# Kernel optimization log

Measured on AMD Instinct MI355X. Metric: run time of the kernel, lower is better.

## Reference

```python
import jax, jax.numpy as jnp
import numpy as np

HEADS = 8

def conv1x1(x, w, b=None):
    # x: [b,c,h,w], w: [o,c]
    y = jnp.einsum('bchw,oc->bohw', x, w)
    if b is not None:
        y = y + b[None, :, None, None]
    return y

def dwconv3(x, w):
    # depthwise 3x3, SAME padding; w: [C,1,3,3]
    return jax.lax.conv_general_dilated(
        x, w, window_strides=(1, 1), padding='SAME',
        feature_group_count=x.shape[1],
        dimension_numbers=('NCHW', 'OIHW', 'NCHW'))

def layernorm_c(x, w, b):
    # WithBias LayerNorm over channel dim (torch normalizes last dim of b,(hw),c)
    mu = x.mean(axis=1, keepdims=True)
    var = ((x - mu) ** 2).mean(axis=1, keepdims=True)
    return (x - mu) / jnp.sqrt(var + 1e-5) * w[None, :, None, None] + b[None, :, None, None]

def l2norm_lastdim(x):
    n = jnp.sqrt(jnp.sum(x * x, axis=-1, keepdims=True))
    return x / jnp.maximum(n, 1e-12)

def channel_attention(xq, xkv, q_w, q_dw_w, kv_w, kv_dw_w, temperature, attn4, proj_w):
    b, c, h, w = xq.shape
    q = dwconv3(conv1x1(xq, q_w), q_dw_w)
    kv = dwconv3(conv1x1(xkv, kv_w), kv_dw_w)
    k, v = jnp.split(kv, 2, axis=1)
    ch = c // HEADS  # channels per head
    def heads(t):
        return t.reshape(b, HEADS, ch, h * w)
    q, k, v = heads(q), heads(k), heads(v)
    q = l2norm_lastdim(q)
    k = l2norm_lastdim(k)
    attn = jnp.einsum('bhcn,bhdn->bhcd', q, k) * temperature[None]  # [b,H,ch,ch]
    kk = int(ch * 0.9)
    thr = jax.lax.top_k(attn, kk)[0][..., -1:]
    masked = jnp.where(attn >= thr, attn, -jnp.inf)
    score = jax.nn.softmax(masked, axis=-1)
    out = jnp.einsum('bhcd,bhdn->bhcn', score, v) * attn4
    out = out.reshape(b, c, h, w)
    return conv1x1(out, proj_w)

def geglu_ffn(x, ffn_in_w, ffn_dw_w, ffn_out_w):
    y = conv1x1(x, ffn_in_w)
    y = dwconv3(y, ffn_dw_w)
    y1, y2 = jnp.split(y, 2, axis=1)
    return conv1x1(jax.nn.gelu(y1, approximate=False) * y2, ffn_out_w)


def reference(vi_featur, ir_featur, text_code,
              se_w1, se_w2, conv1x1_w, conv1x1_b, conv_out_w, conv_out_b,
              text_w1, text_b1, text_w2, text_b2,
              norm1_w, norm1_b, norm2_w, norm2_b, norm3_w, norm3_b,
              q_w, q_dw_w, kv_w, kv_dw_w, temperature, attn4, proj_w,
              ffn_in_w, ffn_dw_w, ffn_out_w):
    b, c, h, w = vi_featur.shape
    concat = jnp.concatenate([vi_featur, ir_featur], axis=1)  # [b,2c,h,w]
    squeeze = concat.mean(axis=(2, 3))                         # [b,2c]
    cw = jax.nn.sigmoid(jax.nn.relu(squeeze @ se_w1.T) @ se_w2.T)
    topk = c  # int(2*ch_dim*0.5)
    idx = jax.lax.top_k(cw, topk)[1]                           # [b,topk]
    selected = jnp.take_along_axis(concat, idx[:, :, None, None], axis=1)
    img = conv1x1(selected, conv1x1_w, conv1x1_b)              # [b,2c,h,w]
    tf = jax.nn.relu(text_code @ text_w1.T + text_b1) @ text_w2.T + text_b2  # [b,2c]
    soft_idx = jax.lax.top_k(tf, 2 * c)[1]                     # full descending perm
    shuffled = jnp.take_along_axis(img, soft_idx[:, :, None, None], axis=1)
    q_in = conv1x1(shuffled, conv_out_w, conv_out_b)           # [b,c,h,w]
    img_feature2 = conv1x1(concat, conv_out_w, conv_out_b)
    att = channel_attention(layernorm_c(q_in, norm1_w, norm1_b),
                            layernorm_c(img_feature2, norm2_w, norm2_b),
                            q_w, q_dw_w, kv_w, kv_dw_w, temperature, attn4, proj_w)
    output = att + geglu_ffn(layernorm_c(att, norm3_w, norm3_b), ffn_in_w, ffn_dw_w, ffn_out_w)
    return (output, img_feature2)


def setup_inputs() -> dict:
    key = jax.random.key(0)
    ks = jax.random.split(key, 20)
    B, C, H, W = 4, 128, 128, 128
    s = 0.05
    d = {
        'vi_featur': jax.random.normal(ks[0], (B, C, H, W), jnp.float32),
        'ir_featur': jax.random.normal(ks[1], (B, C, H, W), jnp.float32),
        'text_code': jax.random.normal(ks[2], (B, 512), jnp.float32),
        'se_w1': jax.random.normal(ks[3], (32, 256), jnp.float32) * s,
        'se_w2': jax.random.normal(ks[4], (256, 32), jnp.float32) * s,
        'conv1x1_w': jax.random.normal(ks[5], (256, 128), jnp.float32) * s,
        'conv1x1_b': jnp.zeros((256,), jnp.float32),
        'conv_out_w': jax.random.normal(ks[6], (128, 256), jnp.float32) * s,
        'conv_out_b': jnp.zeros((128,), jnp.float32),
        'text_w1': jax.random.normal(ks[7], (512, 512), jnp.float32) * s,
        'text_b1': jnp.zeros((512,), jnp.float32),
        'text_w2': jax.random.normal(ks[8], (256, 512), jnp.float32) * s,
        'text_b2': jnp.zeros((256,), jnp.float32),
        'norm1_w': jnp.ones((128,), jnp.float32), 'norm1_b': jnp.zeros((128,), jnp.float32),
        'norm2_w': jnp.ones((128,), jnp.float32), 'norm2_b': jnp.zeros((128,), jnp.float32),
        'norm3_w': jnp.ones((128,), jnp.float32), 'norm3_b': jnp.zeros((128,), jnp.float32),
        'q_w': jax.random.normal(ks[9], (128, 128), jnp.float32) * s,
        'q_dw_w': jax.random.normal(ks[10], (128, 1, 3, 3), jnp.float32) * s,
        'kv_w': jax.random.normal(ks[11], (256, 128), jnp.float32) * s,
        'kv_dw_w': jax.random.normal(ks[12], (256, 1, 3, 3), jnp.float32) * s,
        'temperature': jnp.ones((8, 1, 1), jnp.float32),
        'attn4': jnp.ones((1,), jnp.float32) * 0.2,
        'proj_w': jax.random.normal(ks[13], (128, 128), jnp.float32) * s,
        'ffn_in_w': jax.random.normal(ks[14], (680, 128), jnp.float32) * s,
        'ffn_dw_w': jax.random.normal(ks[15], (680, 1, 3, 3), jnp.float32) * s,
        'ffn_out_w': jax.random.normal(ks[16], (128, 340), jnp.float32) * s,
    }
    return d
```

## Files before the change

kernel.cpp:

```cpp
#include <hip/hip_runtime.h>

typedef unsigned short u16;
typedef __attribute__((ext_vector_type(8))) short bf16x8;
typedef __attribute__((ext_vector_type(4))) float f32x4;

#define N_PIX 16384
static constexpr long NP = 4L * 128 * N_PIX;

__device__ __forceinline__ float bf2f(u16 h) {
  unsigned u = ((unsigned)h) << 16; float f; __builtin_memcpy(&f, &u, 4); return f;
}
__device__ __forceinline__ u16 f2bf(float f) {
  unsigned u; __builtin_memcpy(&u, &f, 4);
  u = (u + 0x7fffu + ((u >> 16) & 1u)) >> 16; return (u16)u;
}

__device__ __forceinline__ float blockReduceSum256(float v) {
  #pragma unroll
  for (int o = 32; o > 0; o >>= 1) v += __shfl_down(v, o, 64);
  __shared__ float sw[4];
  int lane = threadIdx.x & 63, w = threadIdx.x >> 6;
  if (lane == 0) sw[w] = v;
  __syncthreads();
  return (threadIdx.x == 0) ? (sw[0] + sw[1] + sw[2] + sw[3]) : 0.f;
}

__global__ __launch_bounds__(256) void wconv5_k(const float* __restrict__ a0, u16* __restrict__ o0, long n0,
                                                const float* __restrict__ a1, u16* __restrict__ o1, long n1,
                                                const float* __restrict__ a2, u16* __restrict__ o2, long n2,
                                                const float* __restrict__ a3, u16* __restrict__ o3, long n3,
                                                const float* __restrict__ a4, u16* __restrict__ o4, long n4) {
  long i = (long)blockIdx.x * 256 + threadIdx.x;
  if (i < n0) o0[i] = f2bf(a0[i]);
  if (i < n1) o1[i] = f2bf(a1[i]);
  if (i < n2) o2[i] = f2bf(a2[i]);
  if (i < n3) o3[i] = f2bf(a3[i]);
  if (i < n4) o4[i] = f2bf(a4[i]);
}

__global__ __launch_bounds__(256) void squeeze_k(const float* __restrict__ vi,
                                                 const float* __restrict__ ir,
                                                 float* __restrict__ sq,
                                                 u16* __restrict__ cbf) {
  int c = blockIdx.x, b = blockIdx.y, tid = threadIdx.x;
  const float* src = (c < 128) ? (vi + ((long)b * 128 + c) * N_PIX)
                               : (ir + ((long)b * 128 + (c - 128)) * N_PIX);
  const f32x4* src4 = (const f32x4*)src;
  u16* dst = cbf + ((long)b * 256 + c) * N_PIX;
  float s = 0.f;
  #pragma unroll
  for (int j = 0; j < 8; ++j) {
    f32x4 v0 = src4[j * 512 + tid * 2];
    f32x4 v1 = src4[j * 512 + tid * 2 + 1];
    s += v0.x + v0.y + v0.z + v0.w + v1.x + v1.y + v1.z + v1.w;
    bf16x8 r;
    r[0] = (short)f2bf(v0.x); r[1] = (short)f2bf(v0.y);
    r[2] = (short)f2bf(v0.z); r[3] = (short)f2bf(v0.w);
    r[4] = (short)f2bf(v1.x); r[5] = (short)f2bf(v1.y);
    r[6] = (short)f2bf(v1.z); r[7] = (short)f2bf(v1.w);
    *(bf16x8*)(dst + j * 2048 + tid * 8) = r;
  }
  float t = blockReduceSum256(s);
  if (tid == 0) sq[b * 256 + c] = t * (1.f / 16384.f);
}

__global__ __launch_bounds__(256) void se_text1_k(const float* __restrict__ sq,
                                                  const float* __restrict__ sew1,
                                                  const float* __restrict__ sew2,
                                                  int* __restrict__ idx,
                                                  const float* __restrict__ tc,
                                                  const float* __restrict__ tw1,
                                                  const float* __restrict__ tb1,
                                                  float* __restrict__ t1f) {
  int b = blockIdx.y, tid = threadIdx.x;
  __shared__ float sm[544];
  if (blockIdx.x == 64) {
    float* s_sq = sm; float* s_h1 = sm + 256; float* s_cw = sm + 288;
    s_sq[tid] = sq[b * 256 + tid];
    __syncthreads();
    if (tid < 32) {
      float s = 0.f;
      for (int c = 0; c < 256; ++c) s += s_sq[c] * sew1[tid * 256 + c];
      s_h1[tid] = fmaxf(s, 0.f);
    }
    __syncthreads();
    {
      float s = 0.f;
      #pragma unroll
      for (int j = 0; j < 32; ++j) s += s_h1[j] * sew2[tid * 32 + j];
      s_cw[tid] = 1.f / (1.f + expf(-s));
    }
    __syncthreads();
    float my = s_cw[tid];
    int rk = 0;
    for (int c = 0; c < 256; ++c) {
      float o = s_cw[c];
      rk += (o > my) || (o == my && c < tid);
    }
    if (rk < 128) idx[b * 128 + rk] = tid;
  } else {
    float* s_tc = sm;
    int j0 = blockIdx.x * 8;
    s_tc[tid] = tc[b * 512 + tid];
    s_tc[tid + 256] = tc[b * 512 + 256 + tid];
    __syncthreads();
    int w = tid >> 6, lane = tid & 63;
    #pragma unroll
    for (int r = 0; r < 2; ++r) {
      int j = j0 + w * 2 + r;
      const float* wr = tw1 + (long)j * 512;
      float s = 0.f;
      #pragma unroll
      for (int k = 0; k < 8; ++k) s += s_tc[lane + k * 64] * wr[lane + k * 64];
      #pragma unroll
      for (int o = 32; o > 0; o >>= 1) s += __shfl_down(s, o, 64);
      if (lane == 0) t1f[b * 512 + j] = fmaxf(s + tb1[j], 0.f);
    }
  }
}

__global__ __launch_bounds__(256) void text2_k(const float* __restrict__ t1f,
                                               const float* __restrict__ tw2,
                                               const float* __restrict__ tb2,
                                               float* __restrict__ tf) {
  int b = blockIdx.y, j0 = blockIdx.x * 8, tid = threadIdx.x;
  __shared__ float s_t1[512];
  s_t1[tid] = t1f[b * 512 + tid];
  s_t1[tid + 256] = t1f[b * 512 + 256 + tid];
  __syncthreads();
  int w = tid >> 6, lane = tid & 63;
  #pragma unroll
  for (int r = 0; r < 2; ++r) {
    int j = j0 + w * 2 + r;
    const float* wr = tw2 + (long)j * 512;
    float s = 0.f;
    #pragma unroll
    for (int k = 0; k < 8; ++k) s += s_t1[lane + k * 64] * wr[lane + k * 64];
    #pragma unroll
    for (int o = 32; o > 0; o >>= 1) s += __shfl_down(s, o, 64);
    if (lane == 0) tf[b * 256 + j] = s + tb2[j];
  }
}

__global__ __launch_bounds__(256) void rank2_k(const float* __restrict__ tf,
                                               int* __restrict__ sidx) {
  int b = blockIdx.x, tid = threadIdx.x;
  __shared__ float s_tf[256];
  s_tf[tid] = tf[b * 256 + tid];
  __syncthreads();
  float my = s_tf[tid];
  int rk = 0;
  for (int c = 0; c < 256; ++c) {
    float o = s_tf[c];
    rk += (o > my) || (o == my && c < tid);
  }
  sidx[b * 256 + rk] = tid;
}

__global__ __launch_bounds__(128) void mcomb_k(const float* __restrict__ w2,
                                               const float* __restrict__ w2b,
                                               const float* __restrict__ w1,
                                               const float* __restrict__ w1b,
                                               const int* __restrict__ idx,
                                               const int* __restrict__ sidx,
                                               u16* __restrict__ mch,
                                               u16* __restrict__ mcl,
                                               float* __restrict__ bcomb) {
  int o = blockIdx.x, b = blockIdx.y, tid = threadIdx.x;
  __shared__ float s_w2[256];
  __shared__ int s_sx[256];
  s_w2[tid] = w2[o * 256 + tid];
  s_w2[tid + 128] = w2[o * 256 + tid + 128];
  s_sx[tid] = sidx[b * 256 + tid] & 255;
  s_sx[tid + 128] = sidx[b * 256 + tid + 128] & 255;
  u16* hrow = mch + ((long)b * 128 + o) * 256;
  u16* lrow = mcl + ((long)b * 128 + o) * 256;
  hrow[tid] = 0; hrow[tid + 128] = 0;
  lrow[tid] = 0; lrow[tid + 128] = 0;
  __syncthreads();
  float s = 0.f;
  for (int j = 0; j < 256; ++j) s += s_w2[j] * w1[s_sx[j] * 128 + tid];
  int cc = idx[b * 128 + tid] & 255;
  u16 hi = f2bf(s);
  hrow[cc] = hi;
  lrow[cc] = f2bf(s - bf2f(hi));
  if (tid == 0) {
    float bb = w2b[o];
    for (int j = 0; j < 256; ++j) bb += s_w2[j] * w1b[s_sx[j]];
    bcomb[b * 128 + o] = bb;
  }
}

__global__ __launch_bounds__(256) void gemm_dual_k(
    const u16* __restrict__ W2b, const float* __restrict__ b2,
    const u16* __restrict__ Mch, const u16* __restrict__ Mcl,
    const float* __restrict__ bc, const u16* __restrict__ Xb,
    float* __restrict__ out1, u16* __restrict__ xqT, u16* __restrict__ xkvT,
    const float* __restrict__ g1, const float* __restrict__ b1,
    const float* __restrict__ g2, const float* __restrict__ b2n) {
  const int N = N_PIX;
  int n0 = blockIdx.x * 64, bz = blockIdx.z, tid = threadIdx.x;
  __shared__ __align__(16) char smem[36864];
  u16* A1  = (u16*)smem;
  u16* A2h = (u16*)(smem + 9216);
  u16* A2l = (u16*)(smem + 18432);
  u16* Xs  = (u16*)(smem + 27648);
  __shared__ float gs1[128], bs1[128], gs2[128], bs2[128];
  if (tid < 128) { gs1[tid] = g1[tid]; bs1[tid] = b1[tid]; gs2[tid] = g2[tid]; bs2[tid] = b2n[tid]; }
  f32x4 acc1[2][4], acc2[2][4];
  #pragma unroll
  for (int ot = 0; ot < 2; ++ot)
    #pragma unroll
    for (int i = 0; i < 4; ++i) { acc1[ot][i] = (f32x4){0,0,0,0}; acc2[ot][i] = (f32x4){0,0,0,0}; }
  int wv = tid >> 6, lane = tid & 63;
  int lr = lane & 15, lkq = (lane >> 4) * 8;
  for (int kt = 0; kt < 4; ++kt) {
    int k0 = kt << 6;
    {
      int n = tid & 63;
      const u16* src = Xb + (long)bz * 256 * N + n0 + n;
      #pragma unroll
      for (int cc = 0; cc < 2; ++cc) {
        int kb = ((tid >> 6) << 3) + cc * 32;
        int k = k0 + kb;
        bf16x8 t;
        #pragma unroll
        for (int i = 0; i < 8; ++i) t[i] = (short)src[(long)(k + i) * N];
        *(bf16x8*)&Xs[n * 72 + kb] = t;
      }
    }
    #pragma unroll
    for (int ot = 0; ot < 2; ++ot) {
      {
        int r = tid >> 2, o = ot * 64 + r;
        #pragma unroll
        for (int cc = 0; cc < 2; ++cc) {
          int col = ((tid & 3) << 3) + cc * 32;
          int k = k0 + col;
          *(bf16x8*)&A1[r * 72 + col] = *(const bf16x8*)(W2b + (long)o * 256 + k);
          *(bf16x8*)&A2h[r * 72 + col] = *(const bf16x8*)(Mch + ((long)bz * 128 + o) * 256 + k);
          *(bf16x8*)&A2l[r * 72 + col] = *(const bf16x8*)(Mcl + ((long)bz * 128 + o) * 256 + k);
        }
      }
      __syncthreads();
      #pragma unroll
      for (int kk = 0; kk < 2; ++kk) {
        int lk = kk * 32 + lkq;
        bf16x8 a1 = *(const bf16x8*)&A1[(wv * 16 + lr) * 72 + lk];
        bf16x8 a2h = *(const bf16x8*)&A2h[(wv * 16 + lr) * 72 + lk];
        bf16x8 a2l = *(const bf16x8*)&A2l[(wv * 16 + lr) * 72 + lk];
        #pragma unroll
        for (int nt = 0; nt < 4; ++nt) {
          bf16x8 bfr = *(const bf16x8*)&Xs[(nt * 16 + lr) * 72 + lk];
          acc1[ot][nt] = __builtin_amdgcn_mfma_f32_16x16x32_bf16(a1, bfr, acc1[ot][nt], 0, 0, 0);
          acc2[ot][nt] = __builtin_amdgcn_mfma_f32_16x16x32_bf16(a2h, bfr, acc2[ot][nt], 0, 0, 0);
          acc2[ot][nt] = __builtin_amdgcn_mfma_f32_16x16x32_bf16(a2l, bfr, acc2[ot][nt], 0, 0, 0);
        }
      }
      __syncthreads();
    }
  }
  float* st1 = (float*)smem;
  #pragma unroll
  for (int ot = 0; ot < 2; ++ot) {
    #pragma unroll
    for (int nt = 0; nt < 4; ++nt)
      #pragma unroll
      for (int r4 = 0; r4 < 4; ++r4) {
        int o_l = wv * 16 + (lane >> 4) * 4 + r4;
        int n_l = nt * 16 + (lane & 15);
        st1[o_l * 68 + n_l] = acc1[ot][nt][r4] + b2[ot * 64 + o_l];
      }
    __syncthreads();
    {
      int row = tid >> 2, colb = (tid & 3) * 16;
      float* dst = out1 + ((long)bz * 128 + ot * 64 + row) * N + n0 + colb;
      #pragma unroll
      for (int j = 0; j < 4; ++j)
        *(f32x4*)(dst + j * 4) = *(f32x4*)&st1[row * 68 + colb + j * 4];
    }
    __syncthreads();
  }
  u16* stq = (u16*)smem;
  #pragma unroll
  for (int ot = 0; ot < 2; ++ot)
    #pragma unroll
    for (int nt = 0; nt < 4; ++nt)
      #pragma unroll
      for (int r4 = 0; r4 < 4; ++r4) {
        int o_a = ot * 64 + wv * 16 + (lane >> 4) * 4 + r4;
        int n_l = nt * 16 + (lane & 15);
        stq[n_l * 136 + o_a] = f2bf(acc2[ot][nt][r4] + bc[bz * 128 + o_a]);
      }
  __syncthreads();
  {
    int n = tid >> 2, c0 = (tid & 3) * 32;
    bf16x8 v[4];
    float sum = 0.f, sq = 0.f;
    #pragma unroll
    for (int j = 0; j < 4; ++j) {
      v[j] = *(const bf16x8*)&stq[n * 136 + c0 + j * 8];
      #pragma unroll
      for (int i = 0; i < 8; ++i) { float f = bf2f((u16)v[j][i]); sum += f; sq += f * f; }
    }
    sum += __shfl_xor(sum, 1, 64); sum += __shfl_xor(sum, 2, 64);
    sq  += __shfl_xor(sq, 1, 64);  sq  += __shfl_xor(sq, 2, 64);
    float mu = sum * (1.f / 128.f);
    float var = sq * (1.f / 128.f) - mu * mu;
    float rs = rsqrtf(fmaxf(var, 0.f) + 1e-5f);
    u16* dst = xqT + ((long)bz * N_PIX + n0 + n) * 128 + c0;
    #pragma unroll
    for (int j = 0; j < 4; ++j) {
      bf16x8 r;
      #pragma unroll
      for (int i = 0; i < 8; ++i) {
        float f = bf2f((u16)v[j][i]);
        r[i] = (short)f2bf((f - mu) * rs * gs1[c0 + j * 8 + i] + bs1[c0 + j * 8 + i]);
      }
      *(bf16x8*)(dst + j * 8) = r;
    }
  }
  __syncthreads();
  #pragma unroll
  for (int ot = 0; ot < 2; ++ot)
    #pragma unroll
    for (int nt = 0; nt < 4; ++nt)
      #pragma unroll
      for (int r4 = 0; r4 < 4; ++r4) {
        int o_a = ot * 64 + wv * 16 + (lane >> 4) * 4 + r4;
        int n_l = nt * 16 + (lane & 15);
        stq[n_l * 136 + o_a] = f2bf(acc1[ot][nt][r4] + b2[o_a]);
      }
  __syncthreads();
  {
    int n = tid >> 2, c0 = (tid & 3) * 32;
    bf16x8 v[4];
    float sum = 0.f, sq = 0.f;
    #pragma unroll
    for (int j = 0; j < 4; ++j) {
      v[j] = *(const bf16x8*)&stq[n * 136 + c0 + j * 8];
      #pragma unroll
      for (int i = 0; i < 8; ++i) { float f = bf2f((u16)v[j][i]); sum += f; sq += f * f; }
    }
    sum += __shfl_xor(sum, 1, 64); sum += __shfl_xor(sum, 2, 64);
    sq  += __shfl_xor(sq, 1, 64);  sq  += __shfl_xor(sq, 2, 64);
    float mu = sum * (1.f / 128.f);
    float var = sq * (1.f / 128.f) - mu * mu;
    float rs = rsqrtf(fmaxf(var, 0.f) + 1e-5f);
    u16* dst = xkvT + ((long)bz * N_PIX + n0 + n) * 128 + c0;
    #pragma unroll
    for (int j = 0; j < 4; ++j) {
      bf16x8 r;
      #pragma unroll
      for (int i = 0; i < 8; ++i) {
        float f = bf2f((u16)v[j][i]);
        r[i] = (short)f2bf((f - mu) * rs * gs2[c0 + j * 8 + i] + bs2[c0 + j * 8 + i]);
      }
      *(bf16x8*)(dst + j * 8) = r;
    }
  }
}

__global__ __launch_bounds__(256) void att_ln_k(
    const u16* __restrict__ Ah, const u16* __restrict__ Alo,
    const u16* __restrict__ V, long v_bstride,
    u16* __restrict__ att, u16* __restrict__ x3T,
    const float* __restrict__ g3, const float* __restrict__ b3) {
  const int N = N_PIX;
  int n0 = blockIdx.x * 64, bz = blockIdx.z, tid = threadIdx.x;
  int wv = tid >> 6, lane = tid & 63;
  int lr = lane & 15, lkq = (lane >> 4) * 8;
  __shared__ __align__(16) u16 Xs[64][136];
  __shared__ __align__(16) u16 As[64][136];
  __shared__ __align__(16) u16 Al[64][136];
  __shared__ float gs[128], bs[128];
  if (tid < 128) { gs[tid] = g3[tid]; bs[tid] = b3[tid]; }
  f32x4 acc[2][4];
  #pragma unroll
  for (int ot = 0; ot < 2; ++ot)
    #pragma unroll
    for (int i = 0; i < 4; ++i) acc[ot][i] = (f32x4){0.f, 0.f, 0.f, 0.f};
  {
    int n = tid & 63;
    const u16* src = V + (long)bz * v_bstride + n0 + n;
    #pragma unroll
    for (int cc = 0; cc < 4; ++cc) {
      int kb = ((tid >> 6) << 3) + cc * 32;
      bf16x8 t;
      #pragma unroll
      for (int i = 0; i < 8; ++i) t[i] = (short)src[(long)(kb + i) * N];
      *(bf16x8*)&Xs[n][kb] = t;
    }
  }
  #pragma unroll
  for (int ot = 0; ot < 2; ++ot) {
    {
      int r = tid >> 2, o = ot * 64 + r;
      #pragma unroll
      for (int cc = 0; cc < 4; ++cc) {
        int col = ((tid & 3) << 3) + cc * 32;
        long base = (long)bz * (128L * 128) + (long)o * 128 + col;
        *(bf16x8*)&As[r][col] = *(const bf16x8*)(Ah + base);
        *(bf16x8*)&Al[r][col] = *(const bf16x8*)(Alo + base);
      }
    }
    __syncthreads();
    #pragma unroll
    for (int kk = 0; kk < 4; ++kk) {
      int lk = kk * 32 + lkq;
      bf16x8 afr = *(const bf16x8*)&As[wv * 16 + lr][lk];
      bf16x8 alr = *(const bf16x8*)&Al[wv * 16 + lr][lk];
      #pragma unroll
      for (int nt = 0; nt < 4; ++nt) {
        bf16x8 bfr = *(const bf16x8*)&Xs[nt * 16 + lr][lk];
        acc[ot][nt] = __builtin_amdgcn_mfma_f32_16x16x32_bf16(afr, bfr, acc[ot][nt], 0, 0, 0);
        acc[ot][nt] = __builtin_amdgcn_mfma_f32_16x16x32_bf16(alr, bfr, acc[ot][nt], 0, 0, 0);
      }
    }
    __syncthreads();
  }
  u16* st = &Xs[0][0];
  #pragma unroll
  for (int ot = 0; ot < 2; ++ot) {
    #pragma unroll
    for (int nt = 0; nt < 4; ++nt)
      #pragma unroll
      for (int r4 = 0; r4 < 4; ++r4) {
        int row = wv * 16 + (lane >> 4) * 4 + r4;
        int col = nt * 16 + (lane & 15);
        st[row * 72 + col] = f2bf(acc[ot][nt][r4]);
      }
    __syncthreads();
    #pragma unroll
    for (int it = 0; it < 2; ++it) {
      int row = (tid >> 3) + it * 32;
      int col = (tid & 7) * 8;
      bf16x8 v = *(bf16x8*)&st[row * 72 + col];
      *(bf16x8*)(att + ((long)bz * 128 + ot * 64 + row) * N + n0 + col) = v;
    }
    __syncthreads();
  }
  u16* stq = &Xs[0][0];
  #pragma unroll
  for (int ot = 0; ot < 2; ++ot)
    #pragma unroll
    for (int nt = 0; nt < 4; ++nt)
      #pragma unroll
      for (int r4 = 0; r4 < 4; ++r4) {
        int o_a = ot * 64 + wv * 16 + (lane >> 4) * 4 + r4;
        int n_l = nt * 16 + (lane & 15);
        stq[n_l * 136 + o_a] = f2bf(acc[ot][nt][r4]);
      }
  __syncthreads();
  {
    int n = tid >> 2, c0 = (tid & 3) * 32;
    bf16x8 v[4];
    float sum = 0.f, sq = 0.f;
    #pragma unroll
    for (int j = 0; j < 4; ++j) {
      v[j] = *(const bf16x8*)&stq[n * 136 + c0 + j * 8];
      #pragma unroll
      for (int i = 0; i < 8; ++i) { float f = bf2f((u16)v[j][i]); sum += f; sq += f * f; }
    }
    sum += __shfl_xor(sum, 1, 64); sum += __shfl_xor(sum, 2, 64);
    sq  += __shfl_xor(sq, 1, 64);  sq  += __shfl_xor(sq, 2, 64);
    float mu = sum * (1.f / 128.f);
    float var = sq * (1.f / 128.f) - mu * mu;
    float rs = rsqrtf(fmaxf(var, 0.f) + 1e-5f);
    u16* dst = x3T + ((long)bz * N_PIX + n0 + n) * 128 + c0;
    #pragma unroll
    for (int j = 0; j < 4; ++j) {
      bf16x8 r;
      #pragma unroll
      for (int i = 0; i < 8; ++i) {
        float f = bf2f((u16)v[j][i]);
        r[i] = (short)f2bf((f - mu) * rs * gs[c0 + j * 8 + i] + bs[c0 + j * 8 + i]);
      }
      *(bf16x8*)(dst + j * 8) = r;
    }
  }
}

template<int AMODE, int RESADD, int OUTF, int XT, int OT>
__global__ __launch_bounds__(256) void gemm_k(
    const u16* __restrict__ Ah, const u16* __restrict__ Alo, long a_bstride,
    const u16* __restrict__ X, long x_bstride,
    const u16* __restrict__ res, long res_bstride,
    void* __restrict__ outv, long out_bstride,
    int O, int K) {
  const int N = N_PIX;
  int n0 = blockIdx.x * 64;
  int o0 = blockIdx.y * 64 * OT;
  int bz = blockIdx.z;
  int tid = threadIdx.x;
  int wv = tid >> 6, lane = tid & 63;
  int lr = lane & 15, lkq = (lane >> 4) * 8;
  __shared__ __align__(16) u16 Xs[64][136];
  __shared__ __align__(16) u16 As[(XT == 3) ? 1 : 64][136];
  f32x4 acc[OT][4];
  #pragma unroll
  for (int ot = 0; ot < OT; ++ot)
    #pragma unroll
    for (int i = 0; i < 4; ++i) acc[ot][i] = (f32x4){0.f, 0.f, 0.f, 0.f};

  if (XT == 3) {
    {
      int n = tid >> 2, koff = (tid & 3) << 5;
      const u16* src = X + (long)bz * x_bstride + (long)(n0 + n) * 128 + koff;
      #pragma unroll
      for (int j = 0; j < 4; ++j)
        *(bf16x8*)&Xs[n][koff + j * 8] = *(const bf16x8*)(src + j * 8);
    }
    __syncthreads();
    #pragma unroll
    for (int ot = 0; ot < OT; ++ot) {
      int oc = o0 + ot * 64 + wv * 16 + lr;
      if (oc > O - 1) oc = O - 1;
      const u16* Arow = Ah + (long)oc * 128;
      bf16x8 afr[4];
      #pragma unroll
      for (int kk = 0; kk < 4; ++kk) afr[kk] = *(const bf16x8*)(Arow + kk * 32 + lkq);
      #pragma unroll
      for (int kk = 0; kk < 4; ++kk) {
        int lk = kk * 32 + lkq;
        #pragma unroll
        for (int nt = 0; nt < 4; ++nt) {
          bf16x8 bfr = *(const bf16x8*)&Xs[nt * 16 + lr][lk];
          acc[ot][nt] = __builtin_amdgcn_mfma_f32_16x16x32_bf16(afr[kk], bfr, acc[ot][nt], 0, 0, 0);
        }
      }
    }
    __syncthreads();
  } else {
    int nk = (K + 127) >> 7;
    for (int kt = 0; kt < nk; ++kt) {
      int k0 = kt << 7;
      {
        int n = tid & 63;
        const u16* src = X + (long)bz * x_bstride + n0 + n;
        #pragma unroll
        for (int cc = 0; cc < 4; ++cc) {
          int kb = ((tid >> 6) << 3) + cc * 32;
          int k = k0 + kb;
          bf16x8 t;
          #pragma unroll
          for (int i = 0; i < 8; ++i)
            t[i] = (short)((k + i < K) ? src[(long)(k + i) * N] : (u16)0);
          *(bf16x8*)&Xs[n][kb] = t;
        }
      }
      #pragma unroll
      for (int ot = 0; ot < OT; ++ot) {
        {
          int r = tid >> 2, o = o0 + ot * 64 + r;
          #pragma unroll
          for (int cc = 0; cc < 4; ++cc) {
            int col = ((tid & 3) << 3) + cc * 32;
            int k = k0 + col;
            bf16x8 t;
            if (o < O && k + 8 <= K) {
              t = *(const bf16x8*)(Ah + (long)o * K + k);
            } else {
              #pragma unroll
              for (int i = 0; i < 8; ++i)
                t[i] = (short)((o < O && k + i < K) ? Ah[(long)o * K + k + i] : (u16)0);
            }
            *(bf16x8*)&As[r][col] = t;
          }
        }
        __syncthreads();
        #pragma unroll
        for (int kk = 0; kk < 4; ++kk) {
          int lk = kk * 32 + lkq;
          bf16x8 afr = *(const bf16x8*)&As[wv * 16 + lr][lk];
          #pragma unroll
          for (int nt = 0; nt < 4; ++nt) {
            bf16x8 bfr = *(const bf16x8*)&Xs[nt * 16 + lr][lk];
            acc[ot][nt] = __builtin_amdgcn_mfma_f32_16x16x32_bf16(afr, bfr, acc[ot][nt], 0, 0, 0);
          }
        }
        __syncthreads();
      }
    }
  }

  #pragma unroll
  for (int ot = 0; ot < OT; ++ot) {
    if (ot > 0) __syncthreads();
    if (OUTF == 0) {
      u16* st = &Xs[0][0];
      #pragma unroll
      for (int nt = 0; nt < 4; ++nt)
        #pragma unroll
        for (int r4 = 0; r4 < 4; ++r4) {
          int row = wv * 16 + (lane >> 4) * 4 + r4;
          int col = nt * 16 + (lane & 15);
          st[row * 72 + col] = f2bf(acc[ot][nt][r4]);
        }
      __syncthreads();
      #pragma unroll
      for (int it = 0; it < 2; ++it) {
        int row = (tid >> 3) + it * 32;
        int col = (tid & 7) * 8;
        int o = o0 + ot * 64 + row;
        if (o < O) {
          bf16x8 v = *(bf16x8*)&st[row * 72 + col];
          *(bf16x8*)((u16*)outv + (long)bz * out_bstride + (long)o * N + n0 + col) = v;
        }
      }
    } else {
      float* st = (float*)&Xs[0][0];
      #pragma unroll
      for (int nt = 0; nt < 4; ++nt)
        #pragma unroll
        for (int r4 = 0; r4 < 4; ++r4) {
          int row = wv * 16 + (lane >> 4) * 4 + r4;
          int col = nt * 16 + (lane & 15);
          st[row * 68 + col] = acc[ot][nt][r4];
        }
      __syncthreads();
      {
        int row = tid >> 2, colb = (tid & 3) * 16;
        int o = o0 + ot * 64 + row;
        if (o < O) {
          float* dst = (float*)outv + (long)bz * out_bstride + (long)o * N + n0 + colb;
          bf16x8 rv0, rv1;
          if (RESADD) {
            const u16* rp = res + (long)bz * res_bstride + (long)o * N + n0 + colb;
            rv0 = *(const bf16x8*)rp;
            rv1 = *(const bf16x8*)(rp + 8);
          }
          #pragma unroll
          for (int j = 0; j < 4; ++j) {
            f32x4 v = *(f32x4*)&st[row * 68 + colb + j * 4];
            if (RESADD) {
              #pragma unroll
              for (int i = 0; i < 4; ++i) {
                int idx = j * 4 + i;
                u16 rr = (u16)((idx < 8) ? rv0[idx] : rv1[idx - 8]);
                v[i] += bf2f(rr);
              }
            }
            *(f32x4*)(dst + j * 4) = v;
          }
        }
      }
    }
  }
}

__global__ __launch_bounds__(256) void dw3t2_k(const u16* __restrict__ inQ,
                                               const float* __restrict__ wQ,
                                               u16* __restrict__ outQ,
                                               const u16* __restrict__ inKV,
                                               const float* __restrict__ wKV,
                                               u16* __restrict__ outKV) {
  int gp = blockIdx.x >> 3, stripe = blockIdx.x & 7, tid = threadIdx.x;
  const u16* in; const float* w; u16* out; int c; long pbase;
  if (gp < 512) { in = inQ;  w = wQ;  out = outQ;  c = gp & 127;  pbase = (long)gp * N_PIX; }
  else { int p2 = gp - 512; in = inKV; w = wKV; out = outKV; c = p2 & 255; pbase = (long)p2 * N_PIX; }
  int y0 = stripe * 16;
  __shared__ __align__(16) u16 tile[18][136];
  for (int v = tid; v < 288; v += 256) {
    int r = v >> 4, col = (v & 15) << 3;
    int y = y0 - 1 + r;
    bf16x8 t;
    #pragma unroll
    for (int i = 0; i < 8; ++i) t[i] = 0;
    if (y >= 0 && y < 128) t = *(const bf16x8*)(in + pbase + y * 128 + col);
    *(bf16x8*)&tile[r][col] = t;
  }
  float wv[9];
  #pragma unroll
  for (int j = 0; j < 9; ++j) wv[j] = w[c * 9 + j];
  __syncthreads();
  int row = tid >> 4, col0 = (tid & 15) << 3;
  float a[3][10];
  #pragma unroll
  for (int dr = 0; dr < 3; ++dr)
    #pragma unroll
    for (int i = 0; i < 10; ++i) {
      int x = col0 - 1 + i;
      a[dr][i] = (x >= 0 && x < 128) ? bf2f(tile[row + dr][x]) : 0.f;
    }
  bf16x8 res;
  #pragma unroll
  for (int j = 0; j < 8; ++j) {
    float s = 0.f;
    #pragma unroll
    for (int dr = 0; dr < 3; ++dr)
      #pragma unroll
      for (int dx = 0; dx < 3; ++dx) s += wv[dr * 3 + dx] * a[dr][j + dx];
    res[j] = (short)f2bf(s);
  }
  *(bf16x8*)(out + pbase + (y0 + row) * 128 + col0) = res;
}

__global__ __launch_bounds__(256) void dw3gelu4_k(const u16* __restrict__ ft,
                                                  const float* __restrict__ w,
                                                  u16* __restrict__ fg) {
  int plane = blockIdx.x >> 3, stripe = blockIdx.x & 7, tid = threadIdx.x;
  int b = plane / 340, c = plane % 340;
  const u16* t1 = ft + ((long)b * 680 + c) * N_PIX;
  const u16* t2 = ft + ((long)b * 680 + 340 + c) * N_PIX;
  u16* g = fg + ((long)b * 340 + c) * N_PIX;
  int y0 = stripe * 16;
  __shared__ __align__(16) u16 ta[18][136];
  __shared__ __align__(16) u16 tb[18][136];
  for (int v = tid; v < 288; v += 256) {
    int r = v >> 4, col = (v & 15) << 3;
    int y = y0 - 1 + r;
    bf16x8 u1, u2;
    #pragma unroll
    for (int i = 0; i < 8; ++i) { u1[i] = 0; u2[i] = 0; }
    if (y >= 0 && y < 128) {
      u1 = *(const bf16x8*)(t1 + y * 128 + col);
      u2 = *(const bf16x8*)(t2 + y * 128 + col);
    }
    *(bf16x8*)&ta[r][col] = u1;
    *(bf16x8*)&tb[r][col] = u2;
  }
  float w1[9], w2[9];
  #pragma unroll
  for (int j = 0; j < 9; ++j) { w1[j] = w[c * 9 + j]; w2[j] = w[(340 + c) * 9 + j]; }
  __syncthreads();
  int row = tid >> 4, col0 = (tid & 15) << 3;
  float a[3][10], bb[3][10];
  #pragma unroll
  for (int dr = 0; dr < 3; ++dr)
    #pragma unroll
    for (int i = 0; i < 10; ++i) {
      int x = col0 - 1 + i;
      bool ok = (x >= 0 && x < 128);
      a[dr][i] = ok ? bf2f(ta[row + dr][x]) : 0.f;
      bb[dr][i] = ok ? bf2f(tb[row + dr][x]) : 0.f;
    }
  bf16x8 res;
  #pragma unroll
  for (int j = 0; j < 8; ++j) {
    float s1 = 0.f, s2 = 0.f;
    #pragma unroll
    for (int dr = 0; dr < 3; ++dr)
      #pragma unroll
      for (int dx = 0; dx < 3; ++dx) {
        s1 += w1[dr * 3 + dx] * a[dr][j + dx];
        s2 += w2[dr * 3 + dx] * bb[dr][j + dx];
      }
    float gl = 0.5f * s1 * (1.f + erff(s1 * 0.70710678118f));
    res[j] = (short)f2bf(gl * s2);
  }
  *(bf16x8*)(g + (y0 + row) * 128 + col0) = res;
}

__global__ __launch_bounds__(256) void rownorm2_k(const u16* __restrict__ q,
                                                  const u16* __restrict__ kv,
                                                  float* __restrict__ qn,
                                                  float* __restrict__ kn) {
  int x = blockIdx.x, b = blockIdx.y, tid = threadIdx.x;
  const u16* src;
  float* dst;
  if (x < 128) { src = q + (long)b * 128 * N_PIX + (long)x * N_PIX; dst = qn + b * 128 + x; }
  else { int r = x - 128; src = kv + (long)b * 256 * N_PIX + (long)r * N_PIX; dst = kn + b * 128 + r; }
  float s = 0.f;
  #pragma unroll
  for (int j = 0; j < 8; ++j) {
    bf16x8 v = *(const bf16x8*)(src + j * 2048 + tid * 8);
    #pragma unroll
    for (int i = 0; i < 8; ++i) { float f = bf2f((u16)v[i]); s += f * f; }
  }
  float t = blockReduceSum256(s);
  if (tid == 0) *dst = sqrtf(t);
}

__global__ __launch_bounds__(256) void attn_part_k(const u16* __restrict__ q,
                                                   const u16* __restrict__ kbase,
                                                   long kbstride,
                                                   float* __restrict__ part) {
  int ch = blockIdx.x, h = blockIdx.y, b = blockIdx.z, tid = threadIdx.x;
  int n0 = ch * 256;
  __shared__ __align__(16) u16 qc[16][280];
  __shared__ __align__(16) u16 kc[16][280];
  #pragma unroll
  for (int j = 0; j < 2; ++j) {
    int v = tid + j * 256;
    int r = v >> 5, col = (v & 31) << 3;
    *(bf16x8*)&qc[r][col] = *(const bf16x8*)(q + ((long)b * 128 + h * 16 + r) * N_PIX + n0 + col);
    *(bf16x8*)&kc[r][col] = *(const bf16x8*)(kbase + (long)b * kbstride + (long)(h * 16 + r) * N_PIX + n0 + col);
  }
  __syncthreads();
  int c = tid >> 4, d = tid & 15;
  float acc = 0.f;
  #pragma unroll 4
  for (int nb = 0; nb < 32; ++nb) {
    bf16x8 qv = *(const bf16x8*)&qc[c][nb * 8];
    bf16x8 kv = *(const bf16x8*)&kc[d][nb * 8];
    #pragma unroll
    for (int i = 0; i < 8; ++i) acc += bf2f((u16)qv[i]) * bf2f((u16)kv[i]);
  }
  part[(long)((((b * 8 + h) * 16 + c) * 16 + d)) * 64 + ch] = acc;
}

__global__ __launch_bounds__(256) void attn_reduce_k(const float* __restrict__ part,
                                                     const float* __restrict__ qn,
                                                     const float* __restrict__ kn,
                                                     const float* __restrict__ temp,
                                                     float* __restrict__ attnm) {
  int idx = blockIdx.x * 256 + threadIdx.x;
  const float* p = part + (long)idx * 64;
  float s = 0.f;
  #pragma unroll
  for (int j = 0; j < 64; ++j) s += p[j];
  int d = idx & 15, c = (idx >> 4) & 15, h = (idx >> 8) & 7, b = idx >> 11;
  float nq = fmaxf(qn[b * 128 + h * 16 + c], 1e-12f);
  float nk = fmaxf(kn[b * 128 + h * 16 + d], 1e-12f);
  attnm[idx] = s / (nq * nk) * temp[h];
}

__global__ __launch_bounds__(128) void score_cmb_k(const float* __restrict__ attnm,
                                                   const float* __restrict__ projw,
                                                   const float* __restrict__ attn4p,
                                                   u16* __restrict__ cmbh,
                                                   u16* __restrict__ cmbl) {
  int b = blockIdx.x, tid = threadIdx.x;
  __shared__ float att_s[2048], score_s[2048];
  for (int i = tid; i < 2048; i += 128) att_s[i] = attnm[(long)b * 2048 + i];
  __syncthreads();
  {
    int h = tid >> 4, c = tid & 15;
    float v[16], t[16];
    #pragma unroll
    for (int d = 0; d < 16; ++d) { v[d] = att_s[(h * 16 + c) * 16 + d]; t[d] = v[d]; }
    float thr = 0.f, M = -1e30f;
    for (int it = 0; it < 14; ++it) {
      float m = -1e30f; int mi = 0;
      #pragma unroll
      for (int d = 0; d < 16; ++d) if (t[d] > m) { m = t[d]; mi = d; }
      if (it == 0) M = m;
      thr = m;
      t[mi] = -1e31f;
    }
    float s = 0.f, e[16];
    #pragma unroll
    for (int d = 0; d < 16; ++d) { e[d] = (v[d] >= thr) ? expf(v[d] - M) : 0.f; s += e[d]; }
    float inv = 1.f / s;
    #pragma unroll
    for (int d = 0; d < 16; ++d) score_s[(h * 16 + c) * 16 + d] = e[d] * inv;
  }
  __syncthreads();
  float a4 = attn4p[0];
  int o = tid;
  for (int hd = 0; hd < 128; ++hd) {
    int h = hd >> 4, d = hd & 15;
    float s = 0.f;
    #pragma unroll
    for (int c = 0; c < 16; ++c)
      s += projw[o * 128 + h * 16 + c] * score_s[(h * 16 + c) * 16 + d];
    float v = a4 * s;
    long oi = ((long)b * 128 + o) * 128 + hd;
    u16 hi = f2bf(v);
    cmbh[oi] = hi;
    cmbl[oi] = f2bf(v - bf2f(hi));
  }
}

extern "C" void kernel_launch(void* const* d_in, const int* in_sizes, int n_in,
                              void* d_out, int out_size, void* d_ws, size_t ws_size,
                              hipStream_t stream) {
  (void)in_sizes; (void)n_in; (void)out_size; (void)ws_size;
  const float* vi        = (const float*)d_in[0];
  const float* ir        = (const float*)d_in[1];
  const float* text_code = (const float*)d_in[2];
  const float* se_w1     = (const float*)d_in[3];
  const float* se_w2     = (const float*)d_in[4];
  const float* conv1x1_w = (const float*)d_in[5];
  const float* conv1x1_b = (const float*)d_in[6];
  const float* conv_out_w= (const float*)d_in[7];
  const float* conv_out_b= (const float*)d_in[8];
  const float* text_w1   = (const float*)d_in[9];
  const float* text_b1   = (const float*)d_in[10];
  const float* text_w2   = (const float*)d_in[11];
  const float* text_b2   = (const float*)d_in[12];
  const float* norm1_w   = (const float*)d_in[13];
  const float* norm1_b   = (const float*)d_in[14];
  const float* norm2_w   = (const float*)d_in[15];
  const float* norm2_b   = (const float*)d_in[16];
  const float* norm3_w   = (const float*)d_in[17];
  const float* norm3_b   = (const float*)d_in[18];
  const float* q_w       = (const float*)d_in[19];
  const float* q_dw_w    = (const float*)d_in[20];
  const float* kv_w      = (const float*)d_in[21];
  const float* kv_dw_w   = (const float*)d_in[22];
  const float* temperature = (const float*)d_in[23];
  const float* attn4     = (const float*)d_in[24];
  const float* proj_w    = (const float*)d_in[25];
  const float* ffn_in_w  = (const float*)d_in[26];
  const float* ffn_dw_w  = (const float*)d_in[27];
  const float* ffn_out_w = (const float*)d_in[28];
  float* out0 = (float*)d_out;
  float* out1 = out0 + NP;

  char* W = (char*)d_ws;
  float* sq_f  = (float*)(W + 0);
  int*   idx_i = (int*)(W + 4096);
  int*   sidx_i= (int*)(W + 6144);
  u16*   Mch   = (u16*)(W + 12288);
  u16*   Mcl   = (u16*)(W + 274432);
  float* bcomb = (float*)(W + 536576);
  float* qn_f  = (float*)(W + 538624);
  float* kn_f  = (float*)(W + 540672);
  float* attnm = (float*)(W + 542720);
  u16*   cmbh  = (u16*)(W + 575488);
  u16*   cmbl  = (u16*)(W + 706560);
  float* t1f   = (float*)(W + 834560);
  float* tf_f  = (float*)(W + 842752);
  u16*   W2b   = (u16*)(W + 846848);
  u16*   qwb   = (u16*)(W + 912384);
  u16*   kvwb  = (u16*)(W + 945152);
  u16*   ffnWb = (u16*)(W + (1 << 20));
  u16*   ffnOb = (u16*)(W + (1 << 20) + 174080);
  u16* S    = (u16*)(W + (2 << 20));
  u16* CC   = S;
  u16* KD   = S + 512L * N_PIX;
  u16* KVD  = S + 1024L * N_PIX;
  u16* CBF  = S + 1024L * N_PIX;
  u16* X3T  = S + 2048L * N_PIX;
  u16* XKVT = S + 2560L * N_PIX;
  u16* FT4  = S + 2560L * N_PIX;
  u16* FG4  = S + 5280L * N_PIX;
  u16* KVT  = (u16*)out0;
  u16* ATT  = KD;

  const long SN = 128L * N_PIX;
  const long SN2 = 256L * N_PIX;

  wconv5_k<<<340, 256, 0, stream>>>(conv_out_w, W2b, 32768, q_w, qwb, 16384,
                                    kv_w, kvwb, 32768, ffn_in_w, ffnWb, 87040,
                                    ffn_out_w, ffnOb, 43520);
  squeeze_k<<<dim3(256, 4), 256, 0, stream>>>(vi, ir, sq_f, CBF);
  se_text1_k<<<dim3(65, 4), 256, 0, stream>>>(sq_f, se_w1, se_w2, idx_i,
                                              text_code, text_w1, text_b1, t1f);
  text2_k<<<dim3(32, 4), 256, 0, stream>>>(t1f, text_w2, text_b2, tf_f);
  rank2_k<<<4, 256, 0, stream>>>(tf_f, sidx_i);
  mcomb_k<<<dim3(128, 4), 128, 0, stream>>>(conv_out_w, conv_out_b, conv1x1_w,
                                            conv1x1_b, idx_i, sidx_i, Mch, Mcl, bcomb);
  gemm_dual_k<<<dim3(256, 1, 4), 256, 0, stream>>>(
      W2b, conv_out_b, Mch, Mcl, bcomb, CBF, out1, CC, XKVT,
      norm1_w, norm1_b, norm2_w, norm2_b);
  gemm_k<2, 0, 0, 3, 2><<<dim3(256, 1, 4), 256, 0, stream>>>(
      qwb, nullptr, 0, CC, SN, nullptr, 0, KD, SN, 128, 128);
  gemm_k<2, 0, 0, 3, 2><<<dim3(256, 2, 4), 256, 0, stream>>>(
      kvwb, nullptr, 0, XKVT, SN, nullptr, 0, KVT, SN2, 256, 128);
  dw3t2_k<<<12288, 256, 0, stream>>>(KD, q_dw_w, CC, KVT, kv_dw_w, KVD);
  rownorm2_k<<<dim3(256, 4), 256, 0, stream>>>(CC, KVD, qn_f, kn_f);
  float* part = (float*)out0;
  attn_part_k<<<dim3(64, 8, 4), 256, 0, stream>>>(CC, KVD, SN2, part);
  attn_reduce_k<<<32, 256, 0, stream>>>(part, qn_f, kn_f, temperature, attnm);
  score_cmb_k<<<4, 128, 0, stream>>>(attnm, proj_w, attn4, cmbh, cmbl);
  att_ln_k<<<dim3(256, 1, 4), 256, 0, stream>>>(
      cmbh, cmbl, KVD + SN, SN2, ATT, X3T, norm3_w, norm3_b);
  gemm_k<2, 0, 0, 3, 2><<<dim3(256, 6, 4), 256, 0, stream>>>(
      ffnWb, nullptr, 0, X3T, SN, nullptr, 0, FT4, 680L * N_PIX, 680, 128);
  dw3gelu4_k<<<10880, 256, 0, stream>>>(FT4, ffn_dw_w, FG4);
  gemm_k<2, 1, 1, 0, 2><<<dim3(256, 1, 4), 256, 0, stream>>>(
      ffnOb, nullptr, 0, FG4, 340L * N_PIX, ATT, SN,
      out0, SN, 128, 340);
}
```

Before: 352.4 us.

## Transpose concat features to pixel-major bf16 in squeeze kernel for coalesced GEMM loads

The squeeze kernel now tiles 64 pixels by 256 channels and transposes them through an XOR-swizzled shared tile. It writes the bf16 concat tensor in pixel-major layout and emits per-tile partial channel sums, which se_text1_k then reduces. gemm_dual_k loads its X operand with contiguous 16-byte vector reads instead of eight strided scalar loads per channel. The cost is an extra shared-memory transpose, a partial-sum buffer placed in the output region, and a 256-step serial reduction in the SE block.

```diff
diff --git a/kernel.cpp b/kernel.cpp
--- a/kernel.cpp
+++ b/kernel.cpp
@@ -38,33 +38,48 @@
   if (i < n4) o4[i] = f2bf(a4[i]);
 }
 
-__global__ __launch_bounds__(256) void squeeze_k(const float* __restrict__ vi,
-                                                 const float* __restrict__ ir,
-                                                 float* __restrict__ sq,
-                                                 u16* __restrict__ cbf) {
-  int c = blockIdx.x, b = blockIdx.y, tid = threadIdx.x;
-  const float* src = (c < 128) ? (vi + ((long)b * 128 + c) * N_PIX)
-                               : (ir + ((long)b * 128 + (c - 128)) * N_PIX);
-  const f32x4* src4 = (const f32x4*)src;
-  u16* dst = cbf + ((long)b * 256 + c) * N_PIX;
-  float s = 0.f;
-  #pragma unroll
-  for (int j = 0; j < 8; ++j) {
-    f32x4 v0 = src4[j * 512 + tid * 2];
-    f32x4 v1 = src4[j * 512 + tid * 2 + 1];
-    s += v0.x + v0.y + v0.z + v0.w + v1.x + v1.y + v1.z + v1.w;
-    bf16x8 r;
-    r[0] = (short)f2bf(v0.x); r[1] = (short)f2bf(v0.y);
-    r[2] = (short)f2bf(v0.z); r[3] = (short)f2bf(v0.w);
-    r[4] = (short)f2bf(v1.x); r[5] = (short)f2bf(v1.y);
-    r[6] = (short)f2bf(v1.z); r[7] = (short)f2bf(v1.w);
-    *(bf16x8*)(dst + j * 2048 + tid * 8) = r;
-  }
-  float t = blockReduceSum256(s);
-  if (tid == 0) sq[b * 256 + c] = t * (1.f / 16384.f);
-}
-
-__global__ __launch_bounds__(256) void se_text1_k(const float* __restrict__ sq,
+__global__ __launch_bounds__(256) void squeezeT_k(const float* __restrict__ vi,
+                                                  const float* __restrict__ ir,
+                                                  float* __restrict__ spart,
+                                                  u16* __restrict__ cbfT) {
+  int t = blockIdx.x, b = blockIdx.y, tid = threadIdx.x;
+  int p0 = t * 64;
+  __shared__ __align__(16) u16 tile[64][272];
+  __shared__ float s_row[256];
+  int r = tid >> 4, l = tid & 15;
+  #pragma unroll
+  for (int it = 0; it < 16; ++it) {
+    int c = it * 16 + r;
+    const float* src = (c < 128) ? (vi + ((long)b * 128 + c) * N_PIX + p0)
+                                 : (ir + ((long)b * 128 + (c - 128)) * N_PIX + p0);
+    f32x4 v = *(const f32x4*)(src + l * 4);
+    float s = v.x + v.y + v.z + v.w;
+    #pragma unroll
+    for (int o = 8; o > 0; o >>= 1) s += __shfl_down(s, o, 16);
+    if (l == 0) s_row[c] = s;
+    #pragma unroll
+    for (int i = 0; i < 4; ++i) {
+      int px = l * 4 + i;
+      int cs = c ^ (((px >> 1) & 7) << 3);
+      float fv = (i == 0) ? v.x : (i == 1) ? v.y : (i == 2) ? v.z : v.w;
+      tile[px][cs] = f2bf(fv);
+    }
+  }
+  __syncthreads();
+  {
+    int px = tid >> 2, c0 = (tid & 3) * 64;
+    int X = ((px >> 1) & 7) << 3;
+    u16* dst = cbfT + ((long)b * N_PIX + p0 + px) * 256 + c0;
+    #pragma unroll
+    for (int j = 0; j < 8; ++j) {
+      bf16x8 v = *(const bf16x8*)&tile[px][(c0 + j * 8) ^ X];
+      *(bf16x8*)(dst + j * 8) = v;
+    }
+    spart[((long)b * 256 + t) * 256 + tid] = s_row[tid];
+  }
+}
+
+__global__ __launch_bounds__(256) void se_text1_k(const float* __restrict__ spart,
                                                   const float* __restrict__ sew1,
                                                   const float* __restrict__ sew2,
                                                   int* __restrict__ idx,
@@ -76,7 +91,12 @@
   __shared__ float sm[544];
   if (blockIdx.x == 64) {
     float* s_sq = sm; float* s_h1 = sm + 256; float* s_cw = sm + 288;
-    s_sq[tid] = sq[b * 256 + tid];
+    {
+      float s = 0.f;
+      const float* pp = spart + (long)b * 65536 + tid;
+      for (int t2 = 0; t2 < 256; ++t2) s += pp[t2 * 256];
+      s_sq[tid] = s * (1.f / 16384.f);
+    }
     __syncthreads();
     if (tid < 32) {
       float s = 0.f;
@@ -194,7 +214,7 @@
 __global__ __launch_bounds__(256) void gemm_dual_k(
     const u16* __restrict__ W2b, const float* __restrict__ b2,
     const u16* __restrict__ Mch, const u16* __restrict__ Mcl,
-    const float* __restrict__ bc, const u16* __restrict__ Xb,
+    const float* __restrict__ bc, const u16* __restrict__ XbT,
     float* __restrict__ out1, u16* __restrict__ xqT, u16* __restrict__ xkvT,
     const float* __restrict__ g1, const float* __restrict__ b1,
     const float* __restrict__ g2, const float* __restrict__ b2n) {
@@ -217,17 +237,10 @@
   for (int kt = 0; kt < 4; ++kt) {
     int k0 = kt << 6;
     {
-      int n = tid & 63;
-      const u16* src = Xb + (long)bz * 256 * N + n0 + n;
-      #pragma unroll
-      for (int cc = 0; cc < 2; ++cc) {
-        int kb = ((tid >> 6) << 3) + cc * 32;
-        int k = k0 + kb;
-        bf16x8 t;
-        #pragma unroll
-        for (int i = 0; i < 8; ++i) t[i] = (short)src[(long)(k + i) * N];
-        *(bf16x8*)&Xs[n * 72 + kb] = t;
-      }
+      int n = tid >> 2, kc = (tid & 3) << 4;
+      const u16* src = XbT + ((long)bz * N + n0 + n) * 256 + k0 + kc;
+      *(bf16x8*)&Xs[n * 72 + kc] = *(const bf16x8*)src;
+      *(bf16x8*)&Xs[n * 72 + kc + 8] = *(const bf16x8*)(src + 8);
     }
     #pragma unroll
     for (int ot = 0; ot < 2; ++ot) {
@@ -900,7 +913,6 @@
   float* out1 = out0 + NP;
 
   char* W = (char*)d_ws;
-  float* sq_f  = (float*)(W + 0);
   int*   idx_i = (int*)(W + 4096);
   int*   sidx_i= (int*)(W + 6144);
   u16*   Mch   = (u16*)(W + 12288);
@@ -922,13 +934,14 @@
   u16* CC   = S;
   u16* KD   = S + 512L * N_PIX;
   u16* KVD  = S + 1024L * N_PIX;
-  u16* CBF  = S + 1024L * N_PIX;
+  u16* CBT  = S + 1024L * N_PIX;
   u16* X3T  = S + 2048L * N_PIX;
   u16* XKVT = S + 2560L * N_PIX;
   u16* FT4  = S + 2560L * N_PIX;
   u16* FG4  = S + 5280L * N_PIX;
   u16* KVT  = (u16*)out0;
   u16* ATT  = KD;
+  float* spart = out0;
 
   const long SN = 128L * N_PIX;
   const long SN2 = 256L * N_PIX;
@@ -936,15 +949,15 @@
   wconv5_k<<<340, 256, 0, stream>>>(conv_out_w, W2b, 32768, q_w, qwb, 16384,
                                     kv_w, kvwb, 32768, ffn_in_w, ffnWb, 87040,
                                     ffn_out_w, ffnOb, 43520);
-  squeeze_k<<<dim3(256, 4), 256, 0, stream>>>(vi, ir, sq_f, CBF);
-  se_text1_k<<<dim3(65, 4), 256, 0, stream>>>(sq_f, se_w1, se_w2, idx_i,
+  squeezeT_k<<<dim3(256, 4), 256, 0, stream>>>(vi, ir, spart, CBT);
+  se_text1_k<<<dim3(65, 4), 256, 0, stream>>>(spart, se_w1, se_w2, idx_i,
                                               text_code, text_w1, text_b1, t1f);
   text2_k<<<dim3(32, 4), 256, 0, stream>>>(t1f, text_w2, text_b2, tf_f);
   rank2_k<<<4, 256, 0, stream>>>(tf_f, sidx_i);
   mcomb_k<<<dim3(128, 4), 128, 0, stream>>>(conv_out_w, conv_out_b, conv1x1_w,
                                             conv1x1_b, idx_i, sidx_i, Mch, Mcl, bcomb);
   gemm_dual_k<<<dim3(256, 1, 4), 256, 0, stream>>>(
-      W2b, conv_out_b, Mch, Mcl, bcomb, CBF, out1, CC, XKVT,
+      W2b, conv_out_b, Mch, Mcl, bcomb, CBT, out1, CC, XKVT,
       norm1_w, norm1_b, norm2_w, norm2_b);
   gemm_k<2, 0, 0, 3, 2><<<dim3(256, 1, 4), 256, 0, stream>>>(
       qwb, nullptr, 0, CC, SN, nullptr, 0, KD, SN, 128, 128);
```

Result: slower. 365.7 us (+3.8%).
